# Kernel optimization log

Hardware: AMD Instinct MI355X
Metric: run time of the kernel (lower is better)

The kernel has to match this reference:

```python
import jax, jax.numpy as jnp
import numpy as np

N_RES = 256
D_PAIR = 128
NUM_HEADS = 16
D_HEAD = 32
D_INNER = NUM_HEADS * D_HEAD  # 512


def setup_inputs() -> dict:
    key = jax.random.key(0)
    ks = jax.random.split(key, 5)
    s_in = 1.0 / np.sqrt(D_PAIR)
    s_out = 1.0 / np.sqrt(D_INNER)
    return {
        "pair_repr": jax.random.normal(ks[0], (N_RES, N_RES, D_PAIR), jnp.float32),
        "Wq": jax.random.normal(ks[1], (D_PAIR, D_INNER), jnp.float32) * s_in,
        "bq": jnp.zeros((D_INNER,), jnp.float32),
        "Wk": jax.random.normal(ks[2], (D_PAIR, D_INNER), jnp.float32) * s_in,
        "bk": jnp.zeros((D_INNER,), jnp.float32),
        "Wv": jax.random.normal(ks[3], (D_PAIR, D_INNER), jnp.float32) * s_in,
        "bv": jnp.zeros((D_INNER,), jnp.float32),
        "Wo": jax.random.normal(ks[4], (D_INNER, D_PAIR), jnp.float32) * s_out,
        "bo": jnp.zeros((D_PAIR,), jnp.float32),
    }


def reference(pair_repr, Wq, bq, Wk, bk, Wv, bv, Wo, bo):
    N = pair_repr.shape[0]
    # Projections -> (N, N, H, Dh)
    q = (pair_repr @ Wq + bq).reshape(N, N, NUM_HEADS, D_HEAD)
    k = (pair_repr @ Wk + bk).reshape(N, N, NUM_HEADS, D_HEAD)
    v = (pair_repr @ Wv + bv).reshape(N, N, NUM_HEADS, D_HEAD)
    # Triangular attention for starting nodes: attend over k index per row i.
    a = jnp.einsum('ijhc,ikhc->ijkh', q, k) / jnp.sqrt(jnp.asarray(D_HEAD, q.dtype))
    # Lower-triangular mask over (j, k), broadcast over (i, h).
    mask = jnp.tril(jnp.ones((N, N), dtype=bool))[None, :, :, None]
    a = jnp.where(mask, a, jnp.asarray(-1e9, a.dtype))
    a = jax.nn.softmax(a, axis=2)
    o = jnp.einsum('ijkh,ikhc->ijhc', a, v).reshape(N, N, D_INNER)
    return pair_repr + (o @ Wo + bo)
```

## Files before the change

kernel.cpp:

```cpp
#include <hip/hip_runtime.h>
#include <hip/hip_bf16.h>

#define NRES 256
#define DPAIR 128
#define NHEADS 16
#define DHEAD 32
#define DINNER 512

typedef unsigned short u16;
typedef __attribute__((ext_vector_type(4))) float f32x4;
typedef __attribute__((ext_vector_type(8))) short s16x8;
typedef __attribute__((ext_vector_type(4))) short s16x4;

#define QSCALE (0.17677669529663687f * 1.4426950408889634f)

__device__ __forceinline__ u16 f32_to_bf16(float f) {
    unsigned int u = __builtin_bit_cast(unsigned int, f);
    unsigned int r = (u + 0x7FFFu + ((u >> 16) & 1u)) >> 16;
    return (u16)r;
}

__device__ __forceinline__ float fast_exp2(float x) {
#if __has_builtin(__builtin_amdgcn_exp2f)
    return __builtin_amdgcn_exp2f(x);
#else
    return exp2f(x);
#endif
}

__device__ __forceinline__ f32x4 mfma_16x16x16_bf16(s16x4 a, s16x4 b, f32x4 c) {
#if __has_builtin(__builtin_amdgcn_mfma_f32_16x16x16bf16_1k)
    return __builtin_amdgcn_mfma_f32_16x16x16bf16_1k(a, b, c, 0, 0, 0);
#elif __has_builtin(__builtin_amdgcn_mfma_f32_16x16x16_bf16)
    return __builtin_amdgcn_mfma_f32_16x16x16_bf16(a, b, c, 0, 0, 0);
#else
    f32x4 d;
    asm volatile("v_mfma_f32_16x16x16_bf16 %0, %1, %2, %3"
                 : "=v"(d) : "v"(a), "v"(b), "v"(c));
    return d;
#endif
}

__device__ __forceinline__ void gll16(const void* g, void* l) {
    __builtin_amdgcn_global_load_lds(
        (__attribute__((address_space(1))) unsigned int*)(uintptr_t)g,
        (__attribute__((address_space(3))) unsigned int*)(unsigned int)(uintptr_t)l,
        16, 0, 0);
}

__global__ __launch_bounds__(256) void prep_pair(const float* __restrict__ pair,
                                                 u16* __restrict__ pairb) {
    const int id = blockIdx.x * 256 + threadIdx.x;
    const float4* s = reinterpret_cast<const float4*>(pair) + (size_t)id * 2;
    const float4 v0 = s[0], v1 = s[1];
    ushort4 lo, hi;
    lo.x = f32_to_bf16(v0.x); lo.y = f32_to_bf16(v0.y);
    lo.z = f32_to_bf16(v0.z); lo.w = f32_to_bf16(v0.w);
    hi.x = f32_to_bf16(v1.x); hi.y = f32_to_bf16(v1.y);
    hi.z = f32_to_bf16(v1.z); hi.w = f32_to_bf16(v1.w);
    ushort4* d = reinterpret_cast<ushort4*>(pairb + (size_t)id * 8);
    d[0] = lo; d[1] = hi;
}

__global__ __launch_bounds__(256) void wconv(const float* __restrict__ Wq,
                                             const float* __restrict__ Wk,
                                             const float* __restrict__ Wv,
                                             const float* __restrict__ Wo,
                                             u16* wq_t, u16* wk_t, u16* wv_t, u16* wo_t) {
    int id = blockIdx.x * 256 + threadIdx.x;
    if (id < 3 * 65536) {
        int m = id / 65536;
        int e = id % 65536;
        int k = e >> 9, n = e & 511;
        const float* W = (m == 0) ? Wq : ((m == 1) ? Wk : Wv);
        u16* Wt = (m == 0) ? wq_t : ((m == 1) ? wk_t : wv_t);
        Wt[n * 128 + k] = f32_to_bf16(W[e]);
    } else {
        int e = id - 3 * 65536;
        int k = e >> 7, n = e & 127;
        wo_t[n * 512 + k] = f32_to_bf16(Wo[e]);
    }
}

__global__ __launch_bounds__(512, 4) void fused_attn(const u16* __restrict__ pairb,
                                                     const u16* __restrict__ wq_t,
                                                     const u16* __restrict__ wk_t,
                                                     const u16* __restrict__ wv_t,
                                                     const float* __restrict__ bq,
                                                     const float* __restrict__ bk,
                                                     const float* __restrict__ bv,
                                                     u16* __restrict__ o_ws) {
    __shared__ u16 wS[3 * 32 * 128];
    __shared__ u16 qS[256 * 32];
    __shared__ u16 kS[256 * 40];
    __shared__ u16 vTS[32 * 264];

    const int bx = ((blockIdx.x & 7) << 9) | (blockIdx.x >> 3);
    const int i = bx >> 4, h = bx & 15;
    const int tid = threadIdx.x;
    const int wave = tid >> 6, lane = tid & 63;
    const int g = lane >> 4, l15 = lane & 15;
    const int j0 = wave * 32;

    for (int it = 0; it < 3; ++it) {
        const int chunk = wave * 3 + it;
        const int m = chunk >> 3;
        const int lc = chunk & 7;
        const u16* Wt = (m == 0) ? wq_t : ((m == 1) ? wk_t : wv_t);
        const int c = lc * 4 + (lane >> 4);
        const int col = (lane & 15) ^ (c & 7);
        gll16((const char*)(Wt + (size_t)(h * 32) * 128) + c * 256 + col * 16,
              (void*)(wS + (m * 32 + lc * 4) * 128));
    }
    s16x8 pf[2][4];
    {
        const u16* prow = pairb + (size_t)(i * 256 + j0 + l15) * 128;
        #pragma unroll
        for (int jf = 0; jf < 2; ++jf)
            #pragma unroll
            for (int kk = 0; kk < 4; ++kk)
                pf[jf][kk] = *reinterpret_cast<const s16x8*>(prow + jf * 16 * 128 + kk * 32 + g * 8);
    }
    __syncthreads();

    {
        f32x4 aq[2][2], ak[2][2], av[2][2];
        #pragma unroll
        for (int a = 0; a < 2; ++a)
            #pragma unroll
            for (int b = 0; b < 2; ++b) {
                aq[a][b] = f32x4{0.f, 0.f, 0.f, 0.f};
                ak[a][b] = f32x4{0.f, 0.f, 0.f, 0.f};
                av[a][b] = f32x4{0.f, 0.f, 0.f, 0.f};
            }
        #pragma unroll
        for (int kk = 0; kk < 4; ++kk) {
            s16x8 wf[3][2];
            #pragma unroll
            for (int m = 0; m < 3; ++m)
                #pragma unroll
                for (int cf = 0; cf < 2; ++cf) {
                    const int c = cf * 16 + l15;
                    const int ch = (kk * 4 + g) ^ (c & 7);
                    wf[m][cf] = *reinterpret_cast<s16x8*>(&wS[(m * 32 + c) * 128 + ch * 8]);
                }
            #pragma unroll
            for (int cf = 0; cf < 2; ++cf)
                #pragma unroll
                for (int jf = 0; jf < 2; ++jf) {
                    aq[cf][jf] = __builtin_amdgcn_mfma_f32_16x16x32_bf16(wf[0][cf], pf[jf][kk], aq[cf][jf], 0, 0, 0);
                    ak[cf][jf] = __builtin_amdgcn_mfma_f32_16x16x32_bf16(wf[1][cf], pf[jf][kk], ak[cf][jf], 0, 0, 0);
                    av[jf][cf] = __builtin_amdgcn_mfma_f32_16x16x32_bf16(pf[jf][kk], wf[2][cf], av[jf][cf], 0, 0, 0);
                }
        }
        #pragma unroll
        for (int cf = 0; cf < 2; ++cf) {
            const int c = cf * 16 + g * 4;
            const float4 b4q = *reinterpret_cast<const float4*>(bq + h * 32 + c);
            const float4 b4k = *reinterpret_cast<const float4*>(bk + h * 32 + c);
            #pragma unroll
            for (int jf = 0; jf < 2; ++jf) {
                const int j = j0 + jf * 16 + l15;
                ushort4 oq, ok;
                oq.x = f32_to_bf16((aq[cf][jf][0] + b4q.x) * QSCALE);
                oq.y = f32_to_bf16((aq[cf][jf][1] + b4q.y) * QSCALE);
                oq.z = f32_to_bf16((aq[cf][jf][2] + b4q.z) * QSCALE);
                oq.w = f32_to_bf16((aq[cf][jf][3] + b4q.w) * QSCALE);
                *reinterpret_cast<ushort4*>(
                    &qS[j * 32 + (((cf << 1) + (g >> 1)) ^ (j & 3)) * 8 + (g & 1) * 4]) = oq;
                ok.x = f32_to_bf16(ak[cf][jf][0] + b4k.x);
                ok.y = f32_to_bf16(ak[cf][jf][1] + b4k.y);
                ok.z = f32_to_bf16(ak[cf][jf][2] + b4k.z);
                ok.w = f32_to_bf16(ak[cf][jf][3] + b4k.w);
                *reinterpret_cast<ushort4*>(&kS[j * 40 + c]) = ok;
            }
        }
        #pragma unroll
        for (int cf = 0; cf < 2; ++cf) {
            const int c = cf * 16 + l15;
            const float bvv = bv[h * 32 + c];
            #pragma unroll
            for (int jf = 0; jf < 2; ++jf) {
                const int j = j0 + jf * 16 + g * 4;
                ushort4 ov;
                ov.x = f32_to_bf16(av[jf][cf][0] + bvv);
                ov.y = f32_to_bf16(av[jf][cf][1] + bvv);
                ov.z = f32_to_bf16(av[jf][cf][2] + bvv);
                ov.w = f32_to_bf16(av[jf][cf][3] + bvv);
                *reinterpret_cast<ushort4*>(&vTS[c * 264 + j]) = ov;
            }
        }
    }
    __syncthreads();

    const size_t obase = ((size_t)i * 256) * 512 + h * 32;

    for (int ch2 = 0; ch2 < 2; ++ch2) {
        const int t = (ch2 == 0) ? wave : (15 - wave);
        const int jbase = t * 16;
        const int ktmax = t + 1;

        const s16x8 qf = *reinterpret_cast<const s16x8*>(
            &qS[(jbase + l15) * 32 + (g ^ (l15 & 3)) * 8]);

        f32x4 oA0 = {0.f, 0.f, 0.f, 0.f}, oA1 = {0.f, 0.f, 0.f, 0.f};
        f32x4 oB0 = {0.f, 0.f, 0.f, 0.f}, oB1 = {0.f, 0.f, 0.f, 0.f};
        float sA = 0.f, sB = 0.f;

        auto body = [&](int kt, f32x4& u0, f32x4& u1, float& sm) {
            const s16x8 kf = *reinterpret_cast<s16x8*>(&kS[(kt * 16 + l15) * 40 + g * 8]);
            f32x4 s = __builtin_amdgcn_mfma_f32_16x16x32_bf16(kf, qf, f32x4{0.f, 0.f, 0.f, 0.f}, 0, 0, 0);
            float p0, p1, p2, p3;
            if (kt == t) {
                p0 = ((g * 4 + 0) > l15) ? 0.f : fast_exp2(s[0]);
                p1 = ((g * 4 + 1) > l15) ? 0.f : fast_exp2(s[1]);
                p2 = ((g * 4 + 2) > l15) ? 0.f : fast_exp2(s[2]);
                p3 = ((g * 4 + 3) > l15) ? 0.f : fast_exp2(s[3]);
            } else {
                p0 = fast_exp2(s[0]); p1 = fast_exp2(s[1]);
                p2 = fast_exp2(s[2]); p3 = fast_exp2(s[3]);
            }
            sm += (p0 + p1) + (p2 + p3);
            unsigned e0 = __builtin_bit_cast(unsigned, p0) + 0x8000u;
            unsigned e1 = __builtin_bit_cast(unsigned, p1) + 0x8000u;
            unsigned e2 = __builtin_bit_cast(unsigned, p2) + 0x8000u;
            unsigned e3 = __builtin_bit_cast(unsigned, p3) + 0x8000u;
            uint2 pw;
            pw.x = __builtin_amdgcn_perm(e1, e0, 0x07060302u);
            pw.y = __builtin_amdgcn_perm(e3, e2, 0x07060302u);
            const s16x4 pb = __builtin_bit_cast(s16x4, pw);
            const s16x4 va0 = *reinterpret_cast<s16x4*>(&vTS[l15 * 264 + kt * 16 + g * 4]);
            const s16x4 va1 = *reinterpret_cast<s16x4*>(&vTS[(16 + l15) * 264 + kt * 16 + g * 4]);
            u0 = mfma_16x16x16_bf16(va0, pb, u0);
            u1 = mfma_16x16x16_bf16(va1, pb, u1);
        };

        int kt = 0;
        for (; kt + 2 <= ktmax; kt += 2) {
            body(kt, oA0, oA1, sA);
            body(kt + 1, oB0, oB1, sB);
        }
        if (kt < ktmax) body(kt, oA0, oA1, sA);

        float sum = sA + sB;
        sum += __shfl_xor(sum, 16, 64);
        sum += __shfl_xor(sum, 32, 64);
        const float rinv = 1.0f / sum;
        const f32x4 o0 = oA0 + oB0;
        const f32x4 o1 = oA1 + oB1;

        unsigned x0 = __builtin_bit_cast(unsigned, o0[0] * rinv) + 0x8000u;
        unsigned x1 = __builtin_bit_cast(unsigned, o0[1] * rinv) + 0x8000u;
        unsigned x2 = __builtin_bit_cast(unsigned, o0[2] * rinv) + 0x8000u;
        unsigned x3 = __builtin_bit_cast(unsigned, o0[3] * rinv) + 0x8000u;
        uint2 w0;
        w0.x = __builtin_amdgcn_perm(x1, x0, 0x07060302u);
        w0.y = __builtin_amdgcn_perm(x3, x2, 0x07060302u);
        unsigned y0 = __builtin_bit_cast(unsigned, o1[0] * rinv) + 0x8000u;
        unsigned y1 = __builtin_bit_cast(unsigned, o1[1] * rinv) + 0x8000u;
        unsigned y2 = __builtin_bit_cast(unsigned, o1[2] * rinv) + 0x8000u;
        unsigned y3 = __builtin_bit_cast(unsigned, o1[3] * rinv) + 0x8000u;
        uint2 w1;
        w1.x = __builtin_amdgcn_perm(y1, y0, 0x07060302u);
        w1.y = __builtin_amdgcn_perm(y3, y2, 0x07060302u);

        u16* orow = o_ws + obase + (size_t)(jbase + l15) * 512;
        *reinterpret_cast<uint2*>(orow + g * 4) = w0;
        *reinterpret_cast<uint2*>(orow + 16 + g * 4) = w1;
    }
}

__global__ __launch_bounds__(256) void outproj(const u16* __restrict__ o_ws,
                                               const u16* __restrict__ wo_t,
                                               const float* __restrict__ pair,
                                               const float* __restrict__ bo,
                                               float* __restrict__ out) {
    __shared__ u16 As[64 * 72];
    __shared__ u16 Bs[128 * 72];
    const int tid = threadIdx.x;
    const int m0 = blockIdx.x * 64;
    const int wave = tid >> 6, lane = tid & 63;
    const int g = lane >> 4, l15 = lane & 15;

    f32x4 acc[8];
    for (int c = 0; c < 8; ++c) acc[c] = f32x4{0.f, 0.f, 0.f, 0.f};

    for (int kt = 0; kt < 8; ++kt) {
        __syncthreads();
        for (int it = 0; it < 2; ++it) {
            int L = tid + it * 256;
            int row = L >> 3, seg = L & 7;
            *reinterpret_cast<s16x8*>(&As[row * 72 + seg * 8]) =
                *reinterpret_cast<const s16x8*>(o_ws + (size_t)(m0 + row) * 512 + kt * 64 + seg * 8);
        }
        for (int it = 0; it < 4; ++it) {
            int L = tid + it * 256;
            int n = L >> 3, seg = L & 7;
            *reinterpret_cast<s16x8*>(&Bs[n * 72 + seg * 8]) =
                *reinterpret_cast<const s16x8*>(wo_t + (size_t)n * 512 + kt * 64 + seg * 8);
        }
        __syncthreads();
        for (int kk = 0; kk < 2; ++kk) {
            const s16x8 a = *reinterpret_cast<s16x8*>(&As[(wave * 16 + l15) * 72 + kk * 32 + g * 8]);
            for (int c = 0; c < 8; ++c) {
                const s16x8 b = *reinterpret_cast<s16x8*>(&Bs[(c * 16 + l15) * 72 + kk * 32 + g * 8]);
                acc[c] = __builtin_amdgcn_mfma_f32_16x16x32_bf16(a, b, acc[c], 0, 0, 0);
            }
        }
    }

    for (int c = 0; c < 8; ++c) {
        const int n = c * 16 + l15;
        const float bias = bo[n];
        for (int r = 0; r < 4; ++r) {
            const size_t row = m0 + wave * 16 + g * 4 + r;
            out[row * 128 + n] = acc[c][r] + bias + pair[row * 128 + n];
        }
    }
}

extern "C" void kernel_launch(void* const* d_in, const int* in_sizes, int n_in,
                              void* d_out, int out_size, void* d_ws, size_t ws_size,
                              hipStream_t stream) {
    const float* pair = (const float*)d_in[0];
    const float* Wq = (const float*)d_in[1];
    const float* bq = (const float*)d_in[2];
    const float* Wk = (const float*)d_in[3];
    const float* bk = (const float*)d_in[4];
    const float* Wv = (const float*)d_in[5];
    const float* bv = (const float*)d_in[6];
    const float* Wo = (const float*)d_in[7];
    const float* bo = (const float*)d_in[8];
    float* out = (float*)d_out;

    char* ws = (char*)d_ws;
    u16* o_ws  = (u16*)(ws);
    u16* wq_t  = (u16*)(ws + 67108864);
    u16* wk_t  = wq_t + 65536;
    u16* wv_t  = wk_t + 65536;
    u16* wo_t  = wv_t + 65536;
    u16* pairb = (u16*)(ws + 67108864 + 1048576);

    wconv<<<1024, 256, 0, stream>>>(Wq, Wk, Wv, Wo, wq_t, wk_t, wv_t, wo_t);
    prep_pair<<<4096, 256, 0, stream>>>(pair, pairb);
    fused_attn<<<4096, 512, 0, stream>>>(pairb, wq_t, wk_t, wv_t, bq, bk, bv, o_ws);
    outproj<<<1024, 256, 0, stream>>>(o_ws, wo_t, pair, bo, out);
}
```

Measured before the change: 119.0 us.

## Merge prep kernels and share K/V tile loads across paired query tiles

Combines the weight-conversion and pair-conversion kernels into one launch to remove a kernel launch boundary. In the attention kernel, each wave now processes its two query tiles (t and 15-t) together, so each K and V tile read from shared memory serves both query tiles over the shared prefix. This cuts LDS reads and adds independent MFMA chains for latency hiding, at the cost of more live accumulator registers.

```diff
diff --git a/kernel.cpp b/kernel.cpp
--- a/kernel.cpp
+++ b/kernel.cpp
@@ -48,37 +48,39 @@
         16, 0, 0);
 }
 
-__global__ __launch_bounds__(256) void prep_pair(const float* __restrict__ pair,
-                                                 u16* __restrict__ pairb) {
-    const int id = blockIdx.x * 256 + threadIdx.x;
-    const float4* s = reinterpret_cast<const float4*>(pair) + (size_t)id * 2;
-    const float4 v0 = s[0], v1 = s[1];
-    ushort4 lo, hi;
-    lo.x = f32_to_bf16(v0.x); lo.y = f32_to_bf16(v0.y);
-    lo.z = f32_to_bf16(v0.z); lo.w = f32_to_bf16(v0.w);
-    hi.x = f32_to_bf16(v1.x); hi.y = f32_to_bf16(v1.y);
-    hi.z = f32_to_bf16(v1.z); hi.w = f32_to_bf16(v1.w);
-    ushort4* d = reinterpret_cast<ushort4*>(pairb + (size_t)id * 8);
-    d[0] = lo; d[1] = hi;
-}
-
-__global__ __launch_bounds__(256) void wconv(const float* __restrict__ Wq,
-                                             const float* __restrict__ Wk,
-                                             const float* __restrict__ Wv,
-                                             const float* __restrict__ Wo,
-                                             u16* wq_t, u16* wk_t, u16* wv_t, u16* wo_t) {
-    int id = blockIdx.x * 256 + threadIdx.x;
-    if (id < 3 * 65536) {
-        int m = id / 65536;
-        int e = id % 65536;
-        int k = e >> 9, n = e & 511;
-        const float* W = (m == 0) ? Wq : ((m == 1) ? Wk : Wv);
-        u16* Wt = (m == 0) ? wq_t : ((m == 1) ? wk_t : wv_t);
-        Wt[n * 128 + k] = f32_to_bf16(W[e]);
+__global__ __launch_bounds__(256) void prep_all(const float* __restrict__ Wq,
+                                                const float* __restrict__ Wk,
+                                                const float* __restrict__ Wv,
+                                                const float* __restrict__ Wo,
+                                                const float* __restrict__ pair,
+                                                u16* wq_t, u16* wk_t, u16* wv_t, u16* wo_t,
+                                                u16* __restrict__ pairb) {
+    const int b = blockIdx.x;
+    if (b < 1024) {
+        int id = b * 256 + threadIdx.x;
+        if (id < 3 * 65536) {
+            int m = id / 65536;
+            int e = id % 65536;
+            int k = e >> 9, n = e & 511;
+            const float* W = (m == 0) ? Wq : ((m == 1) ? Wk : Wv);
+            u16* Wt = (m == 0) ? wq_t : ((m == 1) ? wk_t : wv_t);
+            Wt[n * 128 + k] = f32_to_bf16(W[e]);
+        } else {
+            int e = id - 3 * 65536;
+            int k = e >> 7, n = e & 127;
+            wo_t[n * 512 + k] = f32_to_bf16(Wo[e]);
+        }
     } else {
-        int e = id - 3 * 65536;
-        int k = e >> 7, n = e & 127;
-        wo_t[n * 512 + k] = f32_to_bf16(Wo[e]);
+        const int id = (b - 1024) * 256 + threadIdx.x;
+        const float4* s = reinterpret_cast<const float4*>(pair) + (size_t)id * 2;
+        const float4 v0 = s[0], v1 = s[1];
+        ushort4 lo, hi;
+        lo.x = f32_to_bf16(v0.x); lo.y = f32_to_bf16(v0.y);
+        lo.z = f32_to_bf16(v0.z); lo.w = f32_to_bf16(v0.w);
+        hi.x = f32_to_bf16(v1.x); hi.y = f32_to_bf16(v1.y);
+        hi.z = f32_to_bf16(v1.z); hi.w = f32_to_bf16(v1.w);
+        ushort4* d = reinterpret_cast<ushort4*>(pairb + (size_t)id * 8);
+        d[0] = lo; d[1] = hi;
     }
 }
 
@@ -194,61 +196,79 @@
     __syncthreads();
 
     const size_t obase = ((size_t)i * 256) * 512 + h * 32;
-
-    for (int ch2 = 0; ch2 < 2; ++ch2) {
-        const int t = (ch2 == 0) ? wave : (15 - wave);
-        const int jbase = t * 16;
-        const int ktmax = t + 1;
-
-        const s16x8 qf = *reinterpret_cast<const s16x8*>(
-            &qS[(jbase + l15) * 32 + (g ^ (l15 & 3)) * 8]);
-
-        f32x4 oA0 = {0.f, 0.f, 0.f, 0.f}, oA1 = {0.f, 0.f, 0.f, 0.f};
-        f32x4 oB0 = {0.f, 0.f, 0.f, 0.f}, oB1 = {0.f, 0.f, 0.f, 0.f};
-        float sA = 0.f, sB = 0.f;
-
-        auto body = [&](int kt, f32x4& u0, f32x4& u1, float& sm) {
-            const s16x8 kf = *reinterpret_cast<s16x8*>(&kS[(kt * 16 + l15) * 40 + g * 8]);
-            f32x4 s = __builtin_amdgcn_mfma_f32_16x16x32_bf16(kf, qf, f32x4{0.f, 0.f, 0.f, 0.f}, 0, 0, 0);
-            float p0, p1, p2, p3;
-            if (kt == t) {
-                p0 = ((g * 4 + 0) > l15) ? 0.f : fast_exp2(s[0]);
-                p1 = ((g * 4 + 1) > l15) ? 0.f : fast_exp2(s[1]);
-                p2 = ((g * 4 + 2) > l15) ? 0.f : fast_exp2(s[2]);
-                p3 = ((g * 4 + 3) > l15) ? 0.f : fast_exp2(s[3]);
-            } else {
-                p0 = fast_exp2(s[0]); p1 = fast_exp2(s[1]);
-                p2 = fast_exp2(s[2]); p3 = fast_exp2(s[3]);
-            }
-            sm += (p0 + p1) + (p2 + p3);
-            unsigned e0 = __builtin_bit_cast(unsigned, p0) + 0x8000u;
-            unsigned e1 = __builtin_bit_cast(unsigned, p1) + 0x8000u;
-            unsigned e2 = __builtin_bit_cast(unsigned, p2) + 0x8000u;
-            unsigned e3 = __builtin_bit_cast(unsigned, p3) + 0x8000u;
-            uint2 pw;
-            pw.x = __builtin_amdgcn_perm(e1, e0, 0x07060302u);
-            pw.y = __builtin_amdgcn_perm(e3, e2, 0x07060302u);
-            const s16x4 pb = __builtin_bit_cast(s16x4, pw);
-            const s16x4 va0 = *reinterpret_cast<s16x4*>(&vTS[l15 * 264 + kt * 16 + g * 4]);
-            const s16x4 va1 = *reinterpret_cast<s16x4*>(&vTS[(16 + l15) * 264 + kt * 16 + g * 4]);
-            u0 = mfma_16x16x16_bf16(va0, pb, u0);
-            u1 = mfma_16x16x16_bf16(va1, pb, u1);
-        };
-
-        int kt = 0;
-        for (; kt + 2 <= ktmax; kt += 2) {
-            body(kt, oA0, oA1, sA);
-            body(kt + 1, oB0, oB1, sB);
-        }
-        if (kt < ktmax) body(kt, oA0, oA1, sA);
-
-        float sum = sA + sB;
+    const int tA = wave, tB = 15 - wave;
+
+    const s16x8 qfA = *reinterpret_cast<const s16x8*>(
+        &qS[(tA * 16 + l15) * 32 + (g ^ (l15 & 3)) * 8]);
+    const s16x8 qfB = *reinterpret_cast<const s16x8*>(
+        &qS[(tB * 16 + l15) * 32 + (g ^ (l15 & 3)) * 8]);
+
+    f32x4 accA0 = {0.f, 0.f, 0.f, 0.f}, accA1 = {0.f, 0.f, 0.f, 0.f};
+    f32x4 accB0 = {0.f, 0.f, 0.f, 0.f}, accB1 = {0.f, 0.f, 0.f, 0.f};
+    float sumA = 0.f, sumB = 0.f;
+
+    auto rdK = [&](int kt) {
+        return *reinterpret_cast<s16x8*>(&kS[(kt * 16 + l15) * 40 + g * 8]);
+    };
+    auto rdV0 = [&](int kt) {
+        return *reinterpret_cast<s16x4*>(&vTS[l15 * 264 + kt * 16 + g * 4]);
+    };
+    auto rdV1 = [&](int kt) {
+        return *reinterpret_cast<s16x4*>(&vTS[(16 + l15) * 264 + kt * 16 + g * 4]);
+    };
+    auto tile = [&](const s16x8& kf, const s16x4& va0, const s16x4& va1,
+                    const s16x8& qf, f32x4& a0, f32x4& a1, float& sm, bool dg) {
+        f32x4 s = __builtin_amdgcn_mfma_f32_16x16x32_bf16(kf, qf, f32x4{0.f, 0.f, 0.f, 0.f}, 0, 0, 0);
+        float p0, p1, p2, p3;
+        if (dg) {
+            p0 = ((g * 4 + 0) > l15) ? 0.f : fast_exp2(s[0]);
+            p1 = ((g * 4 + 1) > l15) ? 0.f : fast_exp2(s[1]);
+            p2 = ((g * 4 + 2) > l15) ? 0.f : fast_exp2(s[2]);
+            p3 = ((g * 4 + 3) > l15) ? 0.f : fast_exp2(s[3]);
+        } else {
+            p0 = fast_exp2(s[0]); p1 = fast_exp2(s[1]);
+            p2 = fast_exp2(s[2]); p3 = fast_exp2(s[3]);
+        }
+        sm += (p0 + p1) + (p2 + p3);
+        unsigned e0 = __builtin_bit_cast(unsigned, p0) + 0x8000u;
+        unsigned e1 = __builtin_bit_cast(unsigned, p1) + 0x8000u;
+        unsigned e2 = __builtin_bit_cast(unsigned, p2) + 0x8000u;
+        unsigned e3 = __builtin_bit_cast(unsigned, p3) + 0x8000u;
+        uint2 pw;
+        pw.x = __builtin_amdgcn_perm(e1, e0, 0x07060302u);
+        pw.y = __builtin_amdgcn_perm(e3, e2, 0x07060302u);
+        const s16x4 pb = __builtin_bit_cast(s16x4, pw);
+        a0 = mfma_16x16x16_bf16(va0, pb, a0);
+        a1 = mfma_16x16x16_bf16(va1, pb, a1);
+    };
+
+    for (int kt = 0; kt < tA; ++kt) {
+        const s16x8 kf = rdK(kt);
+        const s16x4 v0 = rdV0(kt), v1 = rdV1(kt);
+        tile(kf, v0, v1, qfB, accB0, accB1, sumB, false);
+        tile(kf, v0, v1, qfA, accA0, accA1, sumA, false);
+    }
+    {
+        const s16x8 kf = rdK(tA);
+        const s16x4 v0 = rdV0(tA), v1 = rdV1(tA);
+        tile(kf, v0, v1, qfB, accB0, accB1, sumB, false);
+        tile(kf, v0, v1, qfA, accA0, accA1, sumA, true);
+    }
+    for (int kt = tA + 1; kt < tB; ++kt) {
+        const s16x8 kf = rdK(kt);
+        const s16x4 v0 = rdV0(kt), v1 = rdV1(kt);
+        tile(kf, v0, v1, qfB, accB0, accB1, sumB, false);
+    }
+    {
+        const s16x8 kf = rdK(tB);
+        const s16x4 v0 = rdV0(tB), v1 = rdV1(tB);
+        tile(kf, v0, v1, qfB, accB0, accB1, sumB, true);
+    }
+
+    auto store_o = [&](int jbase, const f32x4& o0, const f32x4& o1, float sum) {
         sum += __shfl_xor(sum, 16, 64);
         sum += __shfl_xor(sum, 32, 64);
         const float rinv = 1.0f / sum;
-        const f32x4 o0 = oA0 + oB0;
-        const f32x4 o1 = oA1 + oB1;
-
         unsigned x0 = __builtin_bit_cast(unsigned, o0[0] * rinv) + 0x8000u;
         unsigned x1 = __builtin_bit_cast(unsigned, o0[1] * rinv) + 0x8000u;
         unsigned x2 = __builtin_bit_cast(unsigned, o0[2] * rinv) + 0x8000u;
@@ -263,11 +283,12 @@
         uint2 w1;
         w1.x = __builtin_amdgcn_perm(y1, y0, 0x07060302u);
         w1.y = __builtin_amdgcn_perm(y3, y2, 0x07060302u);
-
         u16* orow = o_ws + obase + (size_t)(jbase + l15) * 512;
         *reinterpret_cast<uint2*>(orow + g * 4) = w0;
         *reinterpret_cast<uint2*>(orow + 16 + g * 4) = w1;
-    }
+    };
+    store_o(tA * 16, accA0, accA1, sumA);
+    store_o(tB * 16, accB0, accB1, sumB);
 }
 
 __global__ __launch_bounds__(256) void outproj(const u16* __restrict__ o_ws,
@@ -341,8 +362,8 @@
     u16* wo_t  = wv_t + 65536;
     u16* pairb = (u16*)(ws + 67108864 + 1048576);
 
-    wconv<<<1024, 256, 0, stream>>>(Wq, Wk, Wv, Wo, wq_t, wk_t, wv_t, wo_t);
-    prep_pair<<<4096, 256, 0, stream>>>(pair, pairb);
+    prep_all<<<5120, 256, 0, stream>>>(Wq, Wk, Wv, Wo, pair,
+                                       wq_t, wk_t, wv_t, wo_t, pairb);
     fused_attn<<<4096, 512, 0, stream>>>(pairb, wq_t, wk_t, wv_t, bq, bk, bv, o_ws);
     outproj<<<1024, 256, 0, stream>>>(o_ws, wo_t, pair, bo, out);
 }
```

Result: faster. 114.1 us (-4.1%).
